# Performance work log

Hardware: AMD Instinct MI355X
Metric: run time of the kernel (lower is better)

The kernel has to match this reference:

```python
import jax, jax.numpy as jnp
import numpy as np

V, E, H = 256, 16, 10
F2, F3, F4 = 3, 4, 5
CONV_OUT = F2 + F3 + F4  # 12


def setup_inputs() -> dict:
    key = jax.random.key(0)
    ks = jax.random.split(key, 9)
    B, SW, SC = 64, 1024, 20
    inputs = jax.random.randint(ks[0], (B, SW, SC), 0, V, dtype=jnp.int32)
    embeddings = jax.random.normal(ks[1], (V, E), jnp.float32) * 0.1
    kernel2 = jax.random.normal(ks[2], (2, E, 1, F2), jnp.float32) * 0.1
    kernel3 = jax.random.normal(ks[3], (3, E, 1, F3), jnp.float32) * 0.1
    kernel4 = jax.random.normal(ks[4], (4, E, 1, F4), jnp.float32) * 0.1
    # tf.contrib.rnn.LSTMCell: single kernel [input+H, 4H] applied to concat([x, h]), bias [4H]
    w_fw = jax.random.normal(ks[5], (CONV_OUT + H, 4 * H), jnp.float32) * 0.1
    b_fw = jnp.zeros((4 * H,), jnp.float32)
    w_bw = jax.random.normal(ks[6], (CONV_OUT + H, 4 * H), jnp.float32) * 0.1
    b_bw = jnp.zeros((4 * H,), jnp.float32)
    return {"inputs": inputs, "embeddings": embeddings, "kernel2": kernel2,
            "kernel3": kernel3, "kernel4": kernel4, "w_fw": w_fw, "b_fw": b_fw,
            "w_bw": w_bw, "b_bw": b_bw}


def _causal_conv(x, kernel):
    # x: [N, SC, E, 1], kernel: [k, E, 1, f]; left-pad char dim by k-1, valid conv collapses E
    k = kernel.shape[0]
    return jax.lax.conv_general_dilated(
        x, kernel, window_strides=(1, 1),
        padding=[(k - 1, 0), (0, 0)],
        dimension_numbers=("NHWC", "HWIO", "NHWC"))  # -> [N, SC, 1, f]


def _lstm_final_h(seq, W, b):
    # seq: [N, T, D]; returns final hidden state [N, H]. tf gate order: i, j, f, o; forget_bias=1.0
    N = seq.shape[0]
    def step(carry, x_t):
        h, c = carry
        z = jnp.concatenate([x_t, h], axis=-1) @ W + b
        i, j, f, o = jnp.split(z, 4, axis=-1)
        c = jax.nn.sigmoid(f + 1.0) * c + jax.nn.sigmoid(i) * jnp.tanh(j)
        h = jax.nn.sigmoid(o) * jnp.tanh(c)
        return (h, c), None
    init = (jnp.zeros((N, H), seq.dtype), jnp.zeros((N, H), seq.dtype))
    (h, _), _ = jax.lax.scan(step, init, jnp.swapaxes(seq, 0, 1))
    return h


def reference(inputs, embeddings, kernel2, kernel3, kernel4, w_fw, b_fw, w_bw, b_bw):
    B, SW, SC = inputs.shape
    enc = embeddings[inputs]                       # [B, SW, SC, E]
    enc = enc.reshape(B * SW, SC, E, 1)            # [N, SC, E, 1]
    c2 = _causal_conv(enc, kernel2)
    c3 = _causal_conv(enc, kernel3)
    c4 = _causal_conv(enc, kernel4)
    c = jnp.concatenate([c2, c3, c4], axis=3)      # [N, SC, 1, 12]
    c = c.reshape(B * SW, SC, CONV_OUT)
    h_fw = _lstm_final_h(c, w_fw, b_fw)            # forward direction
    h_bw = _lstm_final_h(c[:, ::-1, :], w_bw, b_bw)  # backward direction (reversed seq)
    out = jnp.concatenate([h_fw, h_bw], axis=-1)   # [N, 2H]
    return out.reshape(B, SW, 2 * H)
```

## Files before the change

kernel.cpp:

```cpp
#include <hip/hip_runtime.h>

#define SC 20
#define EDIM 16
#define HDIM 10
#define VOCAB 256
#define SENT VOCAB
#define CROWH 56
#define XROW 24
#define WAVES 4

typedef _Float16 f16;
typedef __attribute__((ext_vector_type(2))) _Float16 f16x2;
typedef __attribute__((ext_vector_type(8))) _Float16 f16x8;
typedef __attribute__((ext_vector_type(4))) float f32x4;

#if __has_builtin(__builtin_amdgcn_exp2f)
#define EXP2F(x) __builtin_amdgcn_exp2f(x)
#else
#define EXP2F(x) exp2f(x)
#endif
#if __has_builtin(__builtin_amdgcn_rcpf)
#define RCPF(x) __builtin_amdgcn_rcpf(x)
#else
#define RCPF(x) (1.0f / (x))
#endif
#define L2E 1.44269504088896340736f

__device__ __forceinline__ float fast_sig(float x) {
    return RCPF(1.0f + EXP2F(-x * L2E));
}
__device__ __forceinline__ float fast_tanh(float x) {
    float e = EXP2F(x * (2.0f * L2E));
    return 1.0f - 2.0f * RCPF(1.0f + e);
}
__device__ __forceinline__ f16x2 bc2(unsigned u) { return __builtin_bit_cast(f16x2, u); }
__device__ __forceinline__ unsigned bcu(f16x2 v) { return __builtin_bit_cast(unsigned, v); }
__device__ __forceinline__ unsigned pk(float a, float b) {
    f16x2 t = {(f16)a, (f16)b};
    return __builtin_bit_cast(unsigned, t);
}

#define G_ISSUE                                                         \
    {   const f16* q0 = &ctab[a0 * CROWH];                              \
        g0a = *(const uint4*)q0;  g0b = *(const uint2*)(q0 + 8);        \
        const f16* q1 = &ctab[a1 * CROWH + 12];                         \
        g1a = *(const uint2*)q1;  g1b = *(const uint2*)(q1 + 4);        \
        g1c = *(const uint2*)(q1 + 8);                                  \
        const f16* q2 = &ctab[a2 * CROWH + 24];                         \
        g2a = *(const uint4*)q2;  g2b = *(const uint2*)(q2 + 8);        \
        const f16* q3 = &ctab[a3 * CROWH + 36];                         \
        g3a = *(const uint2*)q3;  g3b = *(const uint2*)(q3 + 4);        \
        g3c = *(const uint2*)(q3 + 8); }

#define G_SUM                                                           \
    {   f16x2 s0 = bc2(g0a.x) + bc2(g1a.x) + bc2(g2a.x) + bc2(g3a.x);  \
        f16x2 s1 = bc2(g0a.y) + bc2(g1a.y) + bc2(g2a.y) + bc2(g3a.y);  \
        f16x2 s2 = bc2(g0a.z) + bc2(g1b.x) + bc2(g2a.z) + bc2(g3b.x);  \
        f16x2 s3 = bc2(g0a.w) + bc2(g1b.y) + bc2(g2a.w) + bc2(g3b.y);  \
        f16x2 s4 = bc2(g0b.x) + bc2(g1c.x) + bc2(g2b.x) + bc2(g3c.x);  \
        f16x2 s5 = bc2(g0b.y) + bc2(g1c.y) + bc2(g2b.y) + bc2(g3c.y);  \
        xg0 = bcu(s0); xg1 = bcu(s1); xg2 = bcu(s2);                   \
        xg3 = bcu(s3); xg4 = bcu(s4); xg5 = bcu(s5); }

#define G_ADV                                                           \
    if (fw) { a3 = a1; a2 = a0; a1 = chload(pp + 1); a0 = chload(pp + 2); pp += 2; } \
    else    { a0 = a2; a1 = a3; a2 = chload(pp - 4); a3 = chload(pp - 5); pp -= 2; }

__global__ __launch_bounds__(256, 4) void cnn_lstm_kernel(
    const int* __restrict__ inp, const float* __restrict__ emb,
    const float* __restrict__ k2, const float* __restrict__ k3,
    const float* __restrict__ k4,
    const float* __restrict__ wfw, const float* __restrict__ bfw,
    const float* __restrict__ wbw, const float* __restrict__ bbw,
    float* __restrict__ out)
{
    __shared__ __align__(16) f16 ctab[(VOCAB + 1) * CROWH];
    __shared__ __align__(16) f16 xbuf[WAVES][33][XROW];

    const int tid  = threadIdx.x;
    const int lane = tid & 63;
    const int w    = tid >> 6;
    const int g    = lane >> 4;
    const int c16  = lane & 15;
    const int p    = lane >> 5;
    const int s    = lane & 31;

    {
        float er[EDIM];
        const float4* ep = (const float4*)(emb + tid * EDIM);
        float4 e0 = ep[0], e1 = ep[1], e2 = ep[2], e3 = ep[3];
        er[0] = e0.x; er[1] = e0.y; er[2] = e0.z; er[3] = e0.w;
        er[4] = e1.x; er[5] = e1.y; er[6] = e1.z; er[7] = e1.w;
        er[8] = e2.x; er[9] = e2.y; er[10] = e2.z; er[11] = e2.w;
        er[12] = e3.x; er[13] = e3.y; er[14] = e3.z; er[15] = e3.w;

        unsigned wd[24];
        #pragma unroll
        for (int dlt = 0; dlt < 4; ++dlt) {
            float o[12];
            #pragma unroll
            for (int f = 0; f < 12; ++f) o[f] = 0.0f;
            const int tap2 = 1 - dlt, tap3 = 2 - dlt, tap4 = 3 - dlt;
            if (tap2 >= 0) {
                #pragma unroll
                for (int e = 0; e < EDIM; ++e) {
                    const float x = er[e];
                    #pragma unroll
                    for (int f = 0; f < 3; ++f) o[f] += x * k2[(tap2 * EDIM + e) * 3 + f];
                }
            }
            if (tap3 >= 0) {
                #pragma unroll
                for (int e = 0; e < EDIM; ++e) {
                    const float x = er[e];
                    #pragma unroll
                    for (int f = 0; f < 4; ++f) o[3 + f] += x * k3[(tap3 * EDIM + e) * 4 + f];
                }
            }
            {
                #pragma unroll
                for (int e = 0; e < EDIM; ++e) {
                    const float x = er[e];
                    #pragma unroll
                    for (int f = 0; f < 5; ++f) o[7 + f] += x * k4[(tap4 * EDIM + e) * 5 + f];
                }
            }
            #pragma unroll
            for (int k = 0; k < 6; ++k) wd[6 * dlt + k] = pk(o[2 * k], o[2 * k + 1]);
        }
        uint4* dst = (uint4*)&ctab[tid * CROWH];
        #pragma unroll
        for (int j = 0; j < 6; ++j)
            dst[j] = make_uint4(wd[4 * j], wd[4 * j + 1], wd[4 * j + 2], wd[4 * j + 3]);
    }
    if (tid < 6) ((uint4*)&ctab[SENT * CROWH])[tid] = make_uint4(0, 0, 0, 0);

    const int dir   = blockIdx.x >> 9;
    const bool fw   = (dir == 0);
    const int nbase = (blockIdx.x & 511) * 128 + w * 32;
    const int* inp_s = inp + (nbase + s) * SC;
    const float* Wm = fw ? wfw : wbw;
    const float* Bv = fw ? bfw : bbw;

    f16x8 afr[3];
    {
        const int qg = c16 >> 2, r = c16 & 3;
        #pragma unroll
        for (int mg = 0; mg < 3; ++mg) {
            const int Lq = (mg == 0) ? 2 * qg : (mg == 1) ? (2 * qg + 1) : (8 + qg);
            const bool valid = (Lq < HDIM);
            const int lcol = r * HDIM + Lq;
            #pragma unroll
            for (int i = 0; i < 8; ++i) {
                const int kk = 8 * g + i;
                float val = 0.0f;
                if (valid) {
                    if (kk < 22) val = Wm[kk * 40 + lcol];
                    else if (kk == 22) val = Bv[lcol];
                }
                afr[mg][i] = (f16)val;
            }
        }
    }

    if (p == 0) {
        f16* xr = &xbuf[w][s][0];
        *(uint2*)(xr + 12) = make_uint2(0u, 0u);
        *(uint2*)(xr + 16) = make_uint2(0u, 0u);
        *(uint2*)(xr + 20) = make_uint2(0u, pk(1.0f, 0.0f));
    }
    if (lane == 0) {
        uint4* jr = (uint4*)&xbuf[w][32][0];
        jr[0] = make_uint4(0, 0, 0, 0);
        jr[1] = make_uint4(0, 0, 0, 0);
        jr[2] = make_uint4(0, 0, 0, 0);
    }
    __syncthreads();

    auto chload = [&](int q) -> int {
        return ((unsigned)q < (unsigned)SC) ? inp_s[q] : SENT;
    };

    int pp = fw ? p : (SC - 1 - p);
    int a0 = chload(pp), a1 = chload(pp - 1), a2 = chload(pp - 2), a3 = chload(pp - 3);

    unsigned xg0, xg1, xg2, xg3, xg4, xg5;
    uint4 g0a, g2a;
    uint2 g0b, g1a, g1b, g1c, g2b, g3a, g3b, g3c;

    if (p == 0) {
        G_ISSUE
        G_SUM
        f16* xr = &xbuf[w][s][0];
        *(uint4*)xr = make_uint4(xg0, xg1, xg2, xg3);
        *(uint2*)(xr + 8) = make_uint2(xg4, xg5);
        G_ADV
    }

    float creg[2][3], hreg[2][3];
    #pragma unroll
    for (int ms = 0; ms < 2; ++ms)
        #pragma unroll
        for (int mg = 0; mg < 3; ++mg) { creg[ms][mg] = 0.0f; hreg[ms][mg] = 0.0f; }

    const f32x4 zero4 = {0.0f, 0.0f, 0.0f, 0.0f};

    #pragma unroll 1
    for (int t = 0; t < SC; ++t) {
        const bool iswriter = (p == (t & 1));

        if (t > 0 && iswriter) {
            f16* xr = &xbuf[w][s][0];
            *(uint4*)xr = make_uint4(xg0, xg1, xg2, xg3);
            *(uint2*)(xr + 8) = make_uint2(xg4, xg5);
        }

        f16x8 bf0 = *(const f16x8*)&xbuf[w][c16][8 * g];
        f16x8 bf1 = *(const f16x8*)&xbuf[w][16 + c16][8 * g];
        __builtin_amdgcn_sched_barrier(0);

        const bool dogather = (!iswriter) && (t < SC - 1);
        if (dogather) {
            G_ISSUE
            G_ADV
        }
        __builtin_amdgcn_sched_barrier(0);

        f32x4 acc[2][3];
        #pragma unroll
        for (int mg = 0; mg < 3; ++mg) {
            acc[0][mg] = __builtin_amdgcn_mfma_f32_16x16x32_f16(afr[mg], bf0, zero4, 0, 0, 0);
            acc[1][mg] = __builtin_amdgcn_mfma_f32_16x16x32_f16(afr[mg], bf1, zero4, 0, 0, 0);
        }
        __builtin_amdgcn_sched_barrier(0);

        if (dogather) {
            G_SUM
        }

        #pragma unroll
        for (int ms = 0; ms < 2; ++ms) {
            #pragma unroll
            for (int mg = 0; mg < 3; ++mg) {
                const f32x4 z = acc[ms][mg];
                const float ij = fast_sig(z[0]) * fast_tanh(z[1]);
                const float fg = fast_sig(z[2] + 1.0f);
                const float og = fast_sig(z[3]);
                creg[ms][mg] = fg * creg[ms][mg] + ij;
                hreg[ms][mg] = og * fast_tanh(creg[ms][mg]);
            }
            f16* xr = &xbuf[w][16 * ms + c16][0];
            *(unsigned*)(xr + 12 + 2 * g) = pk(hreg[ms][0], hreg[ms][1]);
            if (g < 2) xr[20 + g] = (f16)hreg[ms][2];
        }
        __builtin_amdgcn_sched_barrier(0);
    }

    #pragma unroll
    for (int ms = 0; ms < 2; ++ms) {
        const int n = nbase + 16 * ms + c16;
        float2 hv;
        hv.x = hreg[ms][0];
        hv.y = hreg[ms][1];
        *(float2*)&out[n * (2 * HDIM) + dir * HDIM + 2 * g] = hv;
        if (g < 2) out[n * (2 * HDIM) + dir * HDIM + 8 + g] = hreg[ms][2];
    }
}

extern "C" void kernel_launch(void* const* d_in, const int* in_sizes, int n_in,
                              void* d_out, int out_size, void* d_ws, size_t ws_size,
                              hipStream_t stream) {
    const int*   inp = (const int*)d_in[0];
    const float* emb = (const float*)d_in[1];
    const float* k2  = (const float*)d_in[2];
    const float* k3  = (const float*)d_in[3];
    const float* k4  = (const float*)d_in[4];
    const float* wfw = (const float*)d_in[5];
    const float* bfw = (const float*)d_in[6];
    const float* wbw = (const float*)d_in[7];
    const float* bbw = (const float*)d_in[8];
    float* out = (float*)d_out;

    cnn_lstm_kernel<<<dim3(1024), dim3(256), 0, stream>>>(
        inp, emb, k2, k3, k4, wfw, bfw, wbw, bbw, out);
}
```

Before: 57.41 us.

## Move conv tap summation into MFMA via K=64 and 16 sequences per wave

Drops the f16 VALU summation of the four per-character conv-table slices. The four unsummed 12-wide slices are laid out in the K dimension instead, and the weight matrix is replicated across them so two chained 16x16x32 MFMAs perform both the tap sum and the gate projection. Each wave now processes 16 sequences, one per lane column, with 8 waves per 512-thread block, and each lane gathers one tap slice per step. The aim is shorter per-step serial work and higher occupancy, at the cost of twice the waves and more MFMA K-work per sequence.

Result: slower. 144.8 us (+152.2%).

```diff
diff --git a/kernel.cpp b/kernel.cpp
--- a/kernel.cpp
+++ b/kernel.cpp
@@ -1,13 +1,12 @@
 #include <hip/hip_runtime.h>
 
 #define SC 20
-#define EDIM 16
 #define HDIM 10
 #define VOCAB 256
 #define SENT VOCAB
 #define CROWH 56
-#define XROW 24
-#define WAVES 4
+#define XROW 72
+#define WAVES 8
 
 typedef _Float16 f16;
 typedef __attribute__((ext_vector_type(2))) _Float16 f16x2;
@@ -33,40 +32,12 @@
     float e = EXP2F(x * (2.0f * L2E));
     return 1.0f - 2.0f * RCPF(1.0f + e);
 }
-__device__ __forceinline__ f16x2 bc2(unsigned u) { return __builtin_bit_cast(f16x2, u); }
-__device__ __forceinline__ unsigned bcu(f16x2 v) { return __builtin_bit_cast(unsigned, v); }
 __device__ __forceinline__ unsigned pk(float a, float b) {
     f16x2 t = {(f16)a, (f16)b};
     return __builtin_bit_cast(unsigned, t);
 }
 
-#define G_ISSUE                                                         \
-    {   const f16* q0 = &ctab[a0 * CROWH];                              \
-        g0a = *(const uint4*)q0;  g0b = *(const uint2*)(q0 + 8);        \
-        const f16* q1 = &ctab[a1 * CROWH + 12];                         \
-        g1a = *(const uint2*)q1;  g1b = *(const uint2*)(q1 + 4);        \
-        g1c = *(const uint2*)(q1 + 8);                                  \
-        const f16* q2 = &ctab[a2 * CROWH + 24];                         \
-        g2a = *(const uint4*)q2;  g2b = *(const uint2*)(q2 + 8);        \
-        const f16* q3 = &ctab[a3 * CROWH + 36];                         \
-        g3a = *(const uint2*)q3;  g3b = *(const uint2*)(q3 + 4);        \
-        g3c = *(const uint2*)(q3 + 8); }
-
-#define G_SUM                                                           \
-    {   f16x2 s0 = bc2(g0a.x) + bc2(g1a.x) + bc2(g2a.x) + bc2(g3a.x);  \
-        f16x2 s1 = bc2(g0a.y) + bc2(g1a.y) + bc2(g2a.y) + bc2(g3a.y);  \
-        f16x2 s2 = bc2(g0a.z) + bc2(g1b.x) + bc2(g2a.z) + bc2(g3b.x);  \
-        f16x2 s3 = bc2(g0a.w) + bc2(g1b.y) + bc2(g2a.w) + bc2(g3b.y);  \
-        f16x2 s4 = bc2(g0b.x) + bc2(g1c.x) + bc2(g2b.x) + bc2(g3c.x);  \
-        f16x2 s5 = bc2(g0b.y) + bc2(g1c.y) + bc2(g2b.y) + bc2(g3c.y);  \
-        xg0 = bcu(s0); xg1 = bcu(s1); xg2 = bcu(s2);                   \
-        xg3 = bcu(s3); xg4 = bcu(s4); xg5 = bcu(s5); }
-
-#define G_ADV                                                           \
-    if (fw) { a3 = a1; a2 = a0; a1 = chload(pp + 1); a0 = chload(pp + 2); pp += 2; } \
-    else    { a0 = a2; a1 = a3; a2 = chload(pp - 4); a3 = chload(pp - 5); pp -= 2; }
-
-__global__ __launch_bounds__(256, 4) void cnn_lstm_kernel(
+__global__ __launch_bounds__(512, 6) void cnn_lstm_kernel(
     const int* __restrict__ inp, const float* __restrict__ emb,
     const float* __restrict__ k2, const float* __restrict__ k3,
     const float* __restrict__ k4,
@@ -75,74 +46,80 @@
     float* __restrict__ out)
 {
     __shared__ __align__(16) f16 ctab[(VOCAB + 1) * CROWH];
-    __shared__ __align__(16) f16 xbuf[WAVES][33][XROW];
+    __shared__ __align__(16) f16 xbuf[WAVES][16][XROW];
 
     const int tid  = threadIdx.x;
     const int lane = tid & 63;
     const int w    = tid >> 6;
     const int g    = lane >> 4;
     const int c16  = lane & 15;
-    const int p    = lane >> 5;
-    const int s    = lane & 31;
-
-    {
-        float er[EDIM];
-        const float4* ep = (const float4*)(emb + tid * EDIM);
+
+    {
+        const int v  = tid >> 1;
+        const int db = (tid & 1) * 2;
+        float er[16];
+        const float4* ep = (const float4*)(emb + v * 16);
         float4 e0 = ep[0], e1 = ep[1], e2 = ep[2], e3 = ep[3];
-        er[0] = e0.x; er[1] = e0.y; er[2] = e0.z; er[3] = e0.w;
-        er[4] = e1.x; er[5] = e1.y; er[6] = e1.z; er[7] = e1.w;
-        er[8] = e2.x; er[9] = e2.y; er[10] = e2.z; er[11] = e2.w;
-        er[12] = e3.x; er[13] = e3.y; er[14] = e3.z; er[15] = e3.w;
-
-        unsigned wd[24];
+        er[0]=e0.x; er[1]=e0.y; er[2]=e0.z; er[3]=e0.w;
+        er[4]=e1.x; er[5]=e1.y; er[6]=e1.z; er[7]=e1.w;
+        er[8]=e2.x; er[9]=e2.y; er[10]=e2.z; er[11]=e2.w;
+        er[12]=e3.x; er[13]=e3.y; er[14]=e3.z; er[15]=e3.w;
+
         #pragma unroll
-        for (int dlt = 0; dlt < 4; ++dlt) {
+        for (int dd = 0; dd < 2; ++dd) {
+            const int dlt = db + dd;
             float o[12];
             #pragma unroll
             for (int f = 0; f < 12; ++f) o[f] = 0.0f;
             const int tap2 = 1 - dlt, tap3 = 2 - dlt, tap4 = 3 - dlt;
             if (tap2 >= 0) {
                 #pragma unroll
-                for (int e = 0; e < EDIM; ++e) {
+                for (int e = 0; e < 16; ++e) {
                     const float x = er[e];
                     #pragma unroll
-                    for (int f = 0; f < 3; ++f) o[f] += x * k2[(tap2 * EDIM + e) * 3 + f];
+                    for (int f = 0; f < 3; ++f) o[f] += x * k2[(tap2 * 16 + e) * 3 + f];
                 }
             }
             if (tap3 >= 0) {
                 #pragma unroll
-                for (int e = 0; e < EDIM; ++e) {
+                for (int e = 0; e < 16; ++e) {
                     const float x = er[e];
                     #pragma unroll
-                    for (int f = 0; f < 4; ++f) o[3 + f] += x * k3[(tap3 * EDIM + e) * 4 + f];
+                    for (int f = 0; f < 4; ++f) o[3 + f] += x * k3[(tap3 * 16 + e) * 4 + f];
                 }
             }
             {
                 #pragma unroll
-                for (int e = 0; e < EDIM; ++e) {
+                for (int e = 0; e < 16; ++e) {
                     const float x = er[e];
                     #pragma unroll
-                    for (int f = 0; f < 5; ++f) o[7 + f] += x * k4[(tap4 * EDIM + e) * 5 + f];
+                    for (int f = 0; f < 5; ++f) o[7 + f] += x * k4[(tap4 * 16 + e) * 5 + f];
                 }
             }
-            #pragma unroll
-            for (int k = 0; k < 6; ++k) wd[6 * dlt + k] = pk(o[2 * k], o[2 * k + 1]);
-        }
-        uint4* dst = (uint4*)&ctab[tid * CROWH];
-        #pragma unroll
-        for (int j = 0; j < 6; ++j)
-            dst[j] = make_uint4(wd[4 * j], wd[4 * j + 1], wd[4 * j + 2], wd[4 * j + 3]);
-    }
-    if (tid < 6) ((uint4*)&ctab[SENT * CROWH])[tid] = make_uint4(0, 0, 0, 0);
-
-    const int dir   = blockIdx.x >> 9;
-    const bool fw   = (dir == 0);
-    const int nbase = (blockIdx.x & 511) * 128 + w * 32;
-    const int* inp_s = inp + (nbase + s) * SC;
+            uint2* dst = (uint2*)&ctab[v * CROWH + 12 * dlt];
+            dst[0] = make_uint2(pk(o[0], o[1]), pk(o[2], o[3]));
+            dst[1] = make_uint2(pk(o[4], o[5]), pk(o[6], o[7]));
+            dst[2] = make_uint2(pk(o[8], o[9]), pk(o[10], o[11]));
+        }
+    }
+    if (tid < 12) ((uint2*)&ctab[SENT * CROWH])[tid] = make_uint2(0u, 0u);
+
+    if (g == 0) {
+        uint4* hr = (uint4*)&xbuf[w][c16][48];
+        hr[0] = make_uint4(0u, 0u, 0u, 0u);
+        hr[1] = make_uint4(0u, pk(1.0f, 0.0f), 0u, 0u);
+    }
+    __syncthreads();
+
+    const int dir = blockIdx.x >> 9;
+    const bool fw = (dir == 0);
+    const int nbase = (blockIdx.x & 511) * 128 + w * 16;
+    const int n = nbase + c16;
+    const int* inp_n = inp + n * SC;
     const float* Wm = fw ? wfw : wbw;
     const float* Bv = fw ? bfw : bbw;
 
-    f16x8 afr[3];
+    f16x8 afr[3][2];
     {
         const int qg = c16 >> 2, r = c16 & 3;
         #pragma unroll
@@ -151,119 +128,88 @@
             const bool valid = (Lq < HDIM);
             const int lcol = r * HDIM + Lq;
             #pragma unroll
-            for (int i = 0; i < 8; ++i) {
-                const int kk = 8 * g + i;
-                float val = 0.0f;
-                if (valid) {
-                    if (kk < 22) val = Wm[kk * 40 + lcol];
-                    else if (kk == 22) val = Bv[lcol];
-                }
-                afr[mg][i] = (f16)val;
-            }
-        }
-    }
-
-    if (p == 0) {
-        f16* xr = &xbuf[w][s][0];
-        *(uint2*)(xr + 12) = make_uint2(0u, 0u);
-        *(uint2*)(xr + 16) = make_uint2(0u, 0u);
-        *(uint2*)(xr + 20) = make_uint2(0u, pk(1.0f, 0.0f));
-    }
-    if (lane == 0) {
-        uint4* jr = (uint4*)&xbuf[w][32][0];
-        jr[0] = make_uint4(0, 0, 0, 0);
-        jr[1] = make_uint4(0, 0, 0, 0);
-        jr[2] = make_uint4(0, 0, 0, 0);
-    }
-    __syncthreads();
+            for (int seg = 0; seg < 2; ++seg)
+                #pragma unroll
+                for (int i = 0; i < 8; ++i) {
+                    const int k = 32 * seg + 8 * g + i;
+                    float val = 0.0f;
+                    if (valid) {
+                        if (k < 48)       val = Wm[(k % 12) * 40 + lcol];
+                        else if (k < 58)  val = Wm[(k - 36) * 40 + lcol];
+                        else if (k == 58) val = Bv[lcol];
+                    }
+                    afr[mg][seg][i] = (f16)val;
+                }
+        }
+    }
 
     auto chload = [&](int q) -> int {
-        return ((unsigned)q < (unsigned)SC) ? inp_s[q] : SENT;
+        return ((unsigned)q < (unsigned)SC) ? inp_n[q] : SENT;
     };
 
-    int pp = fw ? p : (SC - 1 - p);
-    int a0 = chload(pp), a1 = chload(pp - 1), a2 = chload(pp - 2), a3 = chload(pp - 3);
-
-    unsigned xg0, xg1, xg2, xg3, xg4, xg5;
-    uint4 g0a, g2a;
-    uint2 g0b, g1a, g1b, g1c, g2b, g3a, g3b, g3c;
-
-    if (p == 0) {
-        G_ISSUE
-        G_SUM
-        f16* xr = &xbuf[w][s][0];
-        *(uint4*)xr = make_uint4(xg0, xg1, xg2, xg3);
-        *(uint2*)(xr + 8) = make_uint2(xg4, xg5);
-        G_ADV
-    }
-
-    float creg[2][3], hreg[2][3];
-    #pragma unroll
-    for (int ms = 0; ms < 2; ++ms)
-        #pragma unroll
-        for (int mg = 0; mg < 3; ++mg) { creg[ms][mg] = 0.0f; hreg[ms][mg] = 0.0f; }
-
+    {
+        const int a0 = chload((fw ? 0 : SC - 1) - g);
+        const uint2* src = (const uint2*)&ctab[a0 * CROWH + 12 * g];
+        uint2 p0 = src[0], p1 = src[1], p2 = src[2];
+        uint2* dst = (uint2*)&xbuf[w][c16][12 * g];
+        dst[0] = p0; dst[1] = p1; dst[2] = p2;
+    }
+    int a = chload(fw ? (1 - g) : (SC - 2 - g));
+
+    float creg[3] = {0.0f, 0.0f, 0.0f};
+    float hreg[3] = {0.0f, 0.0f, 0.0f};
     const f32x4 zero4 = {0.0f, 0.0f, 0.0f, 0.0f};
 
     #pragma unroll 1
     for (int t = 0; t < SC; ++t) {
-        const bool iswriter = (p == (t & 1));
-
-        if (t > 0 && iswriter) {
-            f16* xr = &xbuf[w][s][0];
-            *(uint4*)xr = make_uint4(xg0, xg1, xg2, xg3);
-            *(uint2*)(xr + 8) = make_uint2(xg4, xg5);
-        }
-
         f16x8 bf0 = *(const f16x8*)&xbuf[w][c16][8 * g];
-        f16x8 bf1 = *(const f16x8*)&xbuf[w][16 + c16][8 * g];
-        __builtin_amdgcn_sched_barrier(0);
-
-        const bool dogather = (!iswriter) && (t < SC - 1);
-        if (dogather) {
-            G_ISSUE
-            G_ADV
-        }
-        __builtin_amdgcn_sched_barrier(0);
-
-        f32x4 acc[2][3];
-        #pragma unroll
-        for (int mg = 0; mg < 3; ++mg) {
-            acc[0][mg] = __builtin_amdgcn_mfma_f32_16x16x32_f16(afr[mg], bf0, zero4, 0, 0, 0);
-            acc[1][mg] = __builtin_amdgcn_mfma_f32_16x16x32_f16(afr[mg], bf1, zero4, 0, 0, 0);
-        }
-        __builtin_amdgcn_sched_barrier(0);
-
-        if (dogather) {
-            G_SUM
-        }
-
-        #pragma unroll
-        for (int ms = 0; ms < 2; ++ms) {
-            #pragma unroll
-            for (int mg = 0; mg < 3; ++mg) {
-                const f32x4 z = acc[ms][mg];
-                const float ij = fast_sig(z[0]) * fast_tanh(z[1]);
-                const float fg = fast_sig(z[2] + 1.0f);
-                const float og = fast_sig(z[3]);
-                creg[ms][mg] = fg * creg[ms][mg] + ij;
-                hreg[ms][mg] = og * fast_tanh(creg[ms][mg]);
-            }
-            f16* xr = &xbuf[w][16 * ms + c16][0];
-            *(unsigned*)(xr + 12 + 2 * g) = pk(hreg[ms][0], hreg[ms][1]);
-            if (g < 2) xr[20 + g] = (f16)hreg[ms][2];
-        }
-        __builtin_amdgcn_sched_barrier(0);
-    }
-
-    #pragma unroll
-    for (int ms = 0; ms < 2; ++ms) {
-        const int n = nbase + 16 * ms + c16;
+        f16x8 bf1 = *(const f16x8*)&xbuf[w][c16][32 + 8 * g];
+        __builtin_amdgcn_sched_barrier(0);
+
+        const bool dog = (t < SC - 1);
+        uint2 p0, p1, p2;
+        if (dog) {
+            const uint2* src = (const uint2*)&ctab[a * CROWH + 12 * g];
+            p0 = src[0]; p1 = src[1]; p2 = src[2];
+        }
+        a = chload(fw ? (t + 2 - g) : (SC - 3 - t - g));
+        __builtin_amdgcn_sched_barrier(0);
+
+        f32x4 acc0, acc1, acc2;
+        acc0 = __builtin_amdgcn_mfma_f32_16x16x32_f16(afr[0][0], bf0, zero4, 0, 0, 0);
+        acc1 = __builtin_amdgcn_mfma_f32_16x16x32_f16(afr[1][0], bf0, zero4, 0, 0, 0);
+        acc2 = __builtin_amdgcn_mfma_f32_16x16x32_f16(afr[2][0], bf0, zero4, 0, 0, 0);
+        acc0 = __builtin_amdgcn_mfma_f32_16x16x32_f16(afr[0][1], bf1, acc0, 0, 0, 0);
+        acc1 = __builtin_amdgcn_mfma_f32_16x16x32_f16(afr[1][1], bf1, acc1, 0, 0, 0);
+        acc2 = __builtin_amdgcn_mfma_f32_16x16x32_f16(afr[2][1], bf1, acc2, 0, 0, 0);
+        __builtin_amdgcn_sched_barrier(0);
+
+        {
+            const float ij0 = fast_sig(acc0[0]) * fast_tanh(acc0[1]);
+            creg[0] = fast_sig(acc0[2] + 1.0f) * creg[0] + ij0;
+            hreg[0] = fast_sig(acc0[3]) * fast_tanh(creg[0]);
+            const float ij1 = fast_sig(acc1[0]) * fast_tanh(acc1[1]);
+            creg[1] = fast_sig(acc1[2] + 1.0f) * creg[1] + ij1;
+            hreg[1] = fast_sig(acc1[3]) * fast_tanh(creg[1]);
+            const float ij2 = fast_sig(acc2[0]) * fast_tanh(acc2[1]);
+            creg[2] = fast_sig(acc2[2] + 1.0f) * creg[2] + ij2;
+            hreg[2] = fast_sig(acc2[3]) * fast_tanh(creg[2]);
+        }
+        *(unsigned*)&xbuf[w][c16][48 + 2 * g] = pk(hreg[0], hreg[1]);
+        if (g < 2) xbuf[w][c16][56 + g] = (f16)hreg[2];
+        if (dog) {
+            uint2* dst = (uint2*)&xbuf[w][c16][12 * g];
+            dst[0] = p0; dst[1] = p1; dst[2] = p2;
+        }
+        __builtin_amdgcn_sched_barrier(0);
+    }
+
+    {
         float2 hv;
-        hv.x = hreg[ms][0];
-        hv.y = hreg[ms][1];
+        hv.x = hreg[0];
+        hv.y = hreg[1];
         *(float2*)&out[n * (2 * HDIM) + dir * HDIM + 2 * g] = hv;
-        if (g < 2) out[n * (2 * HDIM) + dir * HDIM + 8 + g] = hreg[ms][2];
+        if (g < 2) out[n * (2 * HDIM) + dir * HDIM + 8 + g] = hreg[2];
     }
 }
 
@@ -281,6 +227,6 @@
     const float* bbw = (const float*)d_in[8];
     float* out = (float*)d_out;
 
-    cnn_lstm_kernel<<<dim3(1024), dim3(256), 0, stream>>>(
+    cnn_lstm_kernel<<<dim3(1024), dim3(512), 0, stream>>>(
         inp, emb, k2, k3, k4, wfw, bfw, wbw, bbw, out);
 }
```

## Software-pipeline LSTM half-tiles and fold gate scaling into MFMA weights

Applied to the files above, without the earlier changes.

Restructures the recurrence loop so the two 16-row halves are staggered: the MFMA for one half is issued while the gate math for the other half runs, with gather and commit of conv features moved between the stages. Prescales the weights by -log2e (or -2log2e for the tanh gate) and folds the forget bias into the bias row. This lets the activations use raw exp2 calls and share reciprocals between pairs of gates. It aims to hide MFMA and LDS latency behind transcendental work and to cut VALU instructions. The cost is more complex synchronisation through shared memory, plus some fp16 precision risk from the scaled weights.

Result: faster. 52.67 us (-8.3%).

```diff
diff --git a/kernel.cpp b/kernel.cpp
--- a/kernel.cpp
+++ b/kernel.cpp
@@ -1,7 +1,6 @@
 #include <hip/hip_runtime.h>
 
 #define SC 20
-#define EDIM 16
 #define HDIM 10
 #define VOCAB 256
 #define SENT VOCAB
@@ -26,13 +25,6 @@
 #endif
 #define L2E 1.44269504088896340736f
 
-__device__ __forceinline__ float fast_sig(float x) {
-    return RCPF(1.0f + EXP2F(-x * L2E));
-}
-__device__ __forceinline__ float fast_tanh(float x) {
-    float e = EXP2F(x * (2.0f * L2E));
-    return 1.0f - 2.0f * RCPF(1.0f + e);
-}
 __device__ __forceinline__ f16x2 bc2(unsigned u) { return __builtin_bit_cast(f16x2, u); }
 __device__ __forceinline__ unsigned bcu(f16x2 v) { return __builtin_bit_cast(unsigned, v); }
 __device__ __forceinline__ unsigned pk(float a, float b) {
@@ -66,6 +58,31 @@
     if (fw) { a3 = a1; a2 = a0; a1 = chload(pp + 1); a0 = chload(pp + 2); pp += 2; } \
     else    { a0 = a2; a1 = a3; a2 = chload(pp - 4); a3 = chload(pp - 5); pp -= 2; }
 
+#define X_COMMIT                                                        \
+    {   f16* xr = &xbuf[w][s][0];                                       \
+        *(uint4*)xr = make_uint4(xg0, xg1, xg2, xg3);                   \
+        *(uint2*)(xr + 8) = make_uint2(xg4, xg5); }
+
+__device__ __forceinline__ void combine3(const f32x4* acc, float* cr, float* hr) {
+    #pragma unroll
+    for (int mg = 0; mg < 3; ++mg) {
+        const f32x4 z = acc[mg];
+        const float E0 = EXP2F(z[0]);
+        const float E1 = EXP2F(z[1]);
+        const float R  = RCPF((1.0f + E0) * (1.0f + E1));
+        const float ij = (1.0f - E1) * R;
+        const float E2 = EXP2F(z[2]);
+        const float E3 = EXP2F(z[3]);
+        const float R2 = RCPF((1.0f + E2) * (1.0f + E3));
+        const float fg = (1.0f + E3) * R2;
+        const float og = (1.0f + E2) * R2;
+        cr[mg] = fg * cr[mg] + ij;
+        const float u  = EXP2F(-2.0f * L2E * cr[mg]);
+        const float th = (1.0f - u) * RCPF(1.0f + u);
+        hr[mg] = og * th;
+    }
+}
+
 __global__ __launch_bounds__(256, 4) void cnn_lstm_kernel(
     const int* __restrict__ inp, const float* __restrict__ emb,
     const float* __restrict__ k2, const float* __restrict__ k3,
@@ -86,13 +103,13 @@
     const int s    = lane & 31;
 
     {
-        float er[EDIM];
-        const float4* ep = (const float4*)(emb + tid * EDIM);
+        float er[16];
+        const float4* ep = (const float4*)(emb + tid * 16);
         float4 e0 = ep[0], e1 = ep[1], e2 = ep[2], e3 = ep[3];
-        er[0] = e0.x; er[1] = e0.y; er[2] = e0.z; er[3] = e0.w;
-        er[4] = e1.x; er[5] = e1.y; er[6] = e1.z; er[7] = e1.w;
-        er[8] = e2.x; er[9] = e2.y; er[10] = e2.z; er[11] = e2.w;
-        er[12] = e3.x; er[13] = e3.y; er[14] = e3.z; er[15] = e3.w;
+        er[0]=e0.x; er[1]=e0.y; er[2]=e0.z; er[3]=e0.w;
+        er[4]=e1.x; er[5]=e1.y; er[6]=e1.z; er[7]=e1.w;
+        er[8]=e2.x; er[9]=e2.y; er[10]=e2.z; er[11]=e2.w;
+        er[12]=e3.x; er[13]=e3.y; er[14]=e3.z; er[15]=e3.w;
 
         unsigned wd[24];
         #pragma unroll
@@ -103,26 +120,26 @@
             const int tap2 = 1 - dlt, tap3 = 2 - dlt, tap4 = 3 - dlt;
             if (tap2 >= 0) {
                 #pragma unroll
-                for (int e = 0; e < EDIM; ++e) {
+                for (int e = 0; e < 16; ++e) {
                     const float x = er[e];
                     #pragma unroll
-                    for (int f = 0; f < 3; ++f) o[f] += x * k2[(tap2 * EDIM + e) * 3 + f];
+                    for (int f = 0; f < 3; ++f) o[f] += x * k2[(tap2 * 16 + e) * 3 + f];
                 }
             }
             if (tap3 >= 0) {
                 #pragma unroll
-                for (int e = 0; e < EDIM; ++e) {
+                for (int e = 0; e < 16; ++e) {
                     const float x = er[e];
                     #pragma unroll
-                    for (int f = 0; f < 4; ++f) o[3 + f] += x * k3[(tap3 * EDIM + e) * 4 + f];
+                    for (int f = 0; f < 4; ++f) o[3 + f] += x * k3[(tap3 * 16 + e) * 4 + f];
                 }
             }
             {
                 #pragma unroll
-                for (int e = 0; e < EDIM; ++e) {
+                for (int e = 0; e < 16; ++e) {
                     const float x = er[e];
                     #pragma unroll
-                    for (int f = 0; f < 5; ++f) o[7 + f] += x * k4[(tap4 * EDIM + e) * 5 + f];
+                    for (int f = 0; f < 5; ++f) o[7 + f] += x * k4[(tap4 * 16 + e) * 5 + f];
                 }
             }
             #pragma unroll
@@ -145,6 +162,7 @@
     f16x8 afr[3];
     {
         const int qg = c16 >> 2, r = c16 & 3;
+        const float sc = (r == 1) ? (-2.0f * L2E) : (-L2E);
         #pragma unroll
         for (int mg = 0; mg < 3; ++mg) {
             const int Lq = (mg == 0) ? 2 * qg : (mg == 1) ? (2 * qg + 1) : (8 + qg);
@@ -155,8 +173,9 @@
                 const int kk = 8 * g + i;
                 float val = 0.0f;
                 if (valid) {
-                    if (kk < 22) val = Wm[kk * 40 + lcol];
-                    else if (kk == 22) val = Bv[lcol];
+                    if (kk < 22)       val = Wm[kk * 40 + lcol];
+                    else if (kk == 22) val = Bv[lcol] + ((r == 2) ? 1.0f : 0.0f);
+                    val *= sc;
                 }
                 afr[mg][i] = (f16)val;
             }
@@ -191,79 +210,78 @@
     if (p == 0) {
         G_ISSUE
         G_SUM
-        f16* xr = &xbuf[w][s][0];
-        *(uint4*)xr = make_uint4(xg0, xg1, xg2, xg3);
-        *(uint2*)(xr + 8) = make_uint2(xg4, xg5);
+        X_COMMIT
         G_ADV
-    }
-
-    float creg[2][3], hreg[2][3];
+    } else {
+        G_ISSUE
+        G_ADV
+    }
+
+    float creg0[3] = {0.f, 0.f, 0.f}, hreg0[3] = {0.f, 0.f, 0.f};
+    float creg1[3] = {0.f, 0.f, 0.f}, hreg1[3] = {0.f, 0.f, 0.f};
+    const f32x4 zero4 = {0.0f, 0.0f, 0.0f, 0.0f};
+
+    f32x4 acc0[3], acc1[3];
+    f16x8 bf0 = *(const f16x8*)&xbuf[w][c16][8 * g];
     #pragma unroll
-    for (int ms = 0; ms < 2; ++ms)
-        #pragma unroll
-        for (int mg = 0; mg < 3; ++mg) { creg[ms][mg] = 0.0f; hreg[ms][mg] = 0.0f; }
-
-    const f32x4 zero4 = {0.0f, 0.0f, 0.0f, 0.0f};
+    for (int mg = 0; mg < 3; ++mg)
+        acc0[mg] = __builtin_amdgcn_mfma_f32_16x16x32_f16(afr[mg], bf0, zero4, 0, 0, 0);
+    f16x8 bf1 = *(const f16x8*)&xbuf[w][16 + c16][8 * g];
+    __builtin_amdgcn_sched_barrier(0);
 
     #pragma unroll 1
     for (int t = 0; t < SC; ++t) {
-        const bool iswriter = (p == (t & 1));
-
-        if (t > 0 && iswriter) {
-            f16* xr = &xbuf[w][s][0];
-            *(uint4*)xr = make_uint4(xg0, xg1, xg2, xg3);
-            *(uint2*)(xr + 8) = make_uint2(xg4, xg5);
-        }
-
-        f16x8 bf0 = *(const f16x8*)&xbuf[w][c16][8 * g];
-        f16x8 bf1 = *(const f16x8*)&xbuf[w][16 + c16][8 * g];
-        __builtin_amdgcn_sched_barrier(0);
-
-        const bool dogather = (!iswriter) && (t < SC - 1);
-        if (dogather) {
+        #pragma unroll
+        for (int mg = 0; mg < 3; ++mg)
+            acc1[mg] = __builtin_amdgcn_mfma_f32_16x16x32_f16(afr[mg], bf1, zero4, 0, 0, 0);
+        __builtin_amdgcn_sched_barrier(0);
+
+        combine3(acc0, creg0, hreg0);
+        {
+            f16* xr = &xbuf[w][c16][0];
+            *(unsigned*)(xr + 12 + 2 * g) = pk(hreg0[0], hreg0[1]);
+            if (g < 2) xr[20 + g] = (f16)hreg0[2];
+        }
+        if (t < SC - 1 && p == ((t + 1) & 1)) {
+            G_SUM
+            X_COMMIT
+        }
+        __builtin_amdgcn_sched_barrier(0);
+
+        bf0 = *(const f16x8*)&xbuf[w][c16][8 * g];
+        __builtin_amdgcn_sched_barrier(0);
+
+        combine3(acc1, creg1, hreg1);
+        {
+            f16* xr = &xbuf[w][16 + c16][0];
+            *(unsigned*)(xr + 12 + 2 * g) = pk(hreg1[0], hreg1[1]);
+            if (g < 2) xr[20 + g] = (f16)hreg1[2];
+        }
+        if (t == SC - 1) break;
+        __builtin_amdgcn_sched_barrier(0);
+
+        #pragma unroll
+        for (int mg = 0; mg < 3; ++mg)
+            acc0[mg] = __builtin_amdgcn_mfma_f32_16x16x32_f16(afr[mg], bf0, zero4, 0, 0, 0);
+
+        bf1 = *(const f16x8*)&xbuf[w][16 + c16][8 * g];
+
+        if (t < SC - 2 && p == (t & 1)) {
             G_ISSUE
             G_ADV
         }
         __builtin_amdgcn_sched_barrier(0);
-
-        f32x4 acc[2][3];
-        #pragma unroll
-        for (int mg = 0; mg < 3; ++mg) {
-            acc[0][mg] = __builtin_amdgcn_mfma_f32_16x16x32_f16(afr[mg], bf0, zero4, 0, 0, 0);
-            acc[1][mg] = __builtin_amdgcn_mfma_f32_16x16x32_f16(afr[mg], bf1, zero4, 0, 0, 0);
-        }
-        __builtin_amdgcn_sched_barrier(0);
-
-        if (dogather) {
-            G_SUM
-        }
-
-        #pragma unroll
-        for (int ms = 0; ms < 2; ++ms) {
-            #pragma unroll
-            for (int mg = 0; mg < 3; ++mg) {
-                const f32x4 z = acc[ms][mg];
-                const float ij = fast_sig(z[0]) * fast_tanh(z[1]);
-                const float fg = fast_sig(z[2] + 1.0f);
-                const float og = fast_sig(z[3]);
-                creg[ms][mg] = fg * creg[ms][mg] + ij;
-                hreg[ms][mg] = og * fast_tanh(creg[ms][mg]);
-            }
-            f16* xr = &xbuf[w][16 * ms + c16][0];
-            *(unsigned*)(xr + 12 + 2 * g) = pk(hreg[ms][0], hreg[ms][1]);
-            if (g < 2) xr[20 + g] = (f16)hreg[ms][2];
-        }
-        __builtin_amdgcn_sched_barrier(0);
-    }
-
-    #pragma unroll
-    for (int ms = 0; ms < 2; ++ms) {
-        const int n = nbase + 16 * ms + c16;
-        float2 hv;
-        hv.x = hreg[ms][0];
-        hv.y = hreg[ms][1];
-        *(float2*)&out[n * (2 * HDIM) + dir * HDIM + 2 * g] = hv;
-        if (g < 2) out[n * (2 * HDIM) + dir * HDIM + 8 + g] = hreg[ms][2];
+    }
+
+    {
+        const int n0 = nbase + c16;
+        float2 hv0; hv0.x = hreg0[0]; hv0.y = hreg0[1];
+        *(float2*)&out[n0 * (2 * HDIM) + dir * HDIM + 2 * g] = hv0;
+        if (g < 2) out[n0 * (2 * HDIM) + dir * HDIM + 8 + g] = hreg0[2];
+        const int n1 = nbase + 16 + c16;
+        float2 hv1; hv1.x = hreg1[0]; hv1.y = hreg1[1];
+        *(float2*)&out[n1 * (2 * HDIM) + dir * HDIM + 2 * g] = hv1;
+        if (g < 2) out[n1 * (2 * HDIM) + dir * HDIM + 8 + g] = hreg1[2];
     }
 }
 
```
